# Optimization experiments

Hardware: AMD Instinct MI355X
Metric: run time of the kernel (lower is better)

The kernel has to match this reference:

```python
import jax, jax.numpy as jnp
import numpy as np

INPUT_DIM = 1024
UNITS = 1024

def setup_inputs() -> dict:
    key = jax.random.key(0)
    ks = jax.random.split(key, 7)
    B, S = 4, 2048
    x = jax.random.normal(ks[0], (B, S, INPUT_DIM), dtype=jnp.float32)
    # nn.Linear weights stored as [out, in]; biases [out]
    scale = 1.0 / np.sqrt(INPUT_DIM)
    Wq = jax.random.uniform(ks[1], (UNITS, INPUT_DIM), jnp.float32, -scale, scale)
    bq = jax.random.uniform(ks[2], (UNITS,), jnp.float32, -scale, scale)
    Wk = jax.random.uniform(ks[3], (UNITS, INPUT_DIM), jnp.float32, -scale, scale)
    bk = jax.random.uniform(ks[4], (UNITS,), jnp.float32, -scale, scale)
    Wv = jax.random.uniform(ks[5], (UNITS, INPUT_DIM), jnp.float32, -scale, scale)
    bv = jax.random.uniform(ks[6], (UNITS,), jnp.float32, -scale, scale)
    return {"x": x, "Wq": Wq, "bq": bq, "Wk": Wk, "bk": bk, "Wv": Wv, "bv": bv}

def reference(x, Wq, bq, Wk, bk, Wv, bv):
    # Q/K/V projections: [B,S,D] @ [D,U]
    Q = jnp.einsum('bsd,ud->bsu', x, Wq) + bq
    K = jnp.einsum('bsd,ud->bsu', x, Wk) + bk
    V = jnp.einsum('bsd,ud->bsu', x, Wv) + bv
    scores = jnp.einsum('bqu,bku->bqk', Q, K) / jnp.sqrt(jnp.float32(UNITS))
    attn = jax.nn.softmax(scores, axis=-1)
    return jnp.einsum('bqk,bku->bqu', attn, V)
```

## Files before the change

kernel.cpp:

```cpp
#include <hip/hip_runtime.h>
#include <cstdint>
#include <cstddef>


typedef unsigned short ushort_t;
typedef __attribute__((ext_vector_type(8))) short short8;
typedef __attribute__((ext_vector_type(4))) float f32x4;

#define AS1 __attribute__((address_space(1)))
#define AS3 __attribute__((address_space(3)))

__device__ __forceinline__ ushort_t f2bf(float f) {
    unsigned int u = __float_as_uint(f);
    u += 0x7FFFu + ((u >> 16) & 1u);
    return (ushort_t)(u >> 16);
}
__device__ __forceinline__ float bf2f(ushort_t b) {
    return __uint_as_float(((unsigned)b) << 16);
}

__device__ __forceinline__ void async_ld16(const void* g, unsigned lds_off) {
    __builtin_amdgcn_global_load_lds((const AS1 void*)(uintptr_t)g,
                                     (AS3 void*)(uintptr_t)lds_off,
                                     16, 0, 0);
}

template <int N>
__device__ __forceinline__ void wait_vmcnt() {
    if constexpr (N == 0)      asm volatile("s_waitcnt vmcnt(0)" ::: "memory");
    else if constexpr (N == 4) asm volatile("s_waitcnt vmcnt(4)" ::: "memory");
    else                       asm volatile("s_waitcnt vmcnt(6)" ::: "memory");
}

template <typename OT, int EPI, int BN>
__global__ __launch_bounds__(512, 2) void gemm8(
    const ushort_t* __restrict__ A, const ushort_t* __restrict__ B,
    const float* __restrict__ bias0, const float* __restrict__ bias1,
    OT* __restrict__ C, int K, int lda, int ldb, int ldc, float scale,
    long long aOffZ, long long bOffZ, long long cOffZ)
{
    constexpr int NJ   = BN / 64;
    constexpr int NBH  = (BN == 256) ? 2 : 1;
    constexpr int VPRO = (BN == 256) ? 6 : 4;

    __shared__ __align__(16) ushort_t As[2][2][128 * 64];
    __shared__ __align__(16) ushort_t Bs[2][NBH][128 * 64];
    __shared__ float rs[256];

    const int tid  = threadIdx.x;
    const int wave = tid >> 6;
    const int lane = tid & 63;

    A += (size_t)blockIdx.z * aOffZ;
    B += (size_t)blockIdx.z * bOffZ;

    const int m0 = blockIdx.y * 256;
    const int n0 = blockIdx.x * BN;
    const int g  = wave >> 2;
    const int wm = g * 128;
    const int wn = (wave & 3) * (BN / 4);

    const int srow = wave * 8 + (lane >> 3);
    const int cd   = ((lane & 7) - srow) & 7;
    const unsigned lw = (unsigned)(wave << 10);

    const ushort_t* Ast = A + (size_t)(m0 + srow) * lda + cd * 8;
    const ushort_t* Bst = B + (size_t)(n0 + srow) * ldb + cd * 8;

    unsigned aB[2][2], bB[2][NBH];
#pragma unroll
    for (int b2 = 0; b2 < 2; ++b2) {
        aB[b2][0] = (unsigned)(uintptr_t)&As[b2][0][0];
        aB[b2][1] = (unsigned)(uintptr_t)&As[b2][1][0];
#pragma unroll
        for (int h = 0; h < NBH; ++h)
            bB[b2][h] = (unsigned)(uintptr_t)&Bs[b2][h][0];
    }

    auto stA = [&](int t, int rsel) {
        const int buf = t & 1;
        const int k0  = t << 6;
        async_ld16(Ast + (size_t)(rsel * 64) * lda + k0,
                   aB[buf][0] + (unsigned)(rsel * 8192) + lw);
        async_ld16(Ast + (size_t)(rsel * 64 + 128) * lda + k0,
                   aB[buf][1] + (unsigned)(rsel * 8192) + lw);
    };
    auto stB = [&](int t, int h) {
        const int buf = t & 1;
        const int k0  = t << 6;
        async_ld16(Bst + (size_t)(h * 128) * ldb + k0, bB[buf][h] + lw);
        async_ld16(Bst + (size_t)(h * 128 + 64) * ldb + k0,
                   bB[buf][h] + 8192 + lw);
    };

    const int frow = lane & 15;
    const int fg   = lane >> 4;
    const int hB   = (BN == 256) ? (wn >> 7) : 0;

    const int NT = K >> 6;

    f32x4 acc[8][NJ] = {};
    float rsacc[8] = {};
    short8 bfr[NJ][2];

    stB(0, 0);
    if (BN == 256) stB(0, 1);
    stA(0, 0); stA(0, 1);
    stB(1, 0);
    if (BN == 256) stB(1, 1);
    stA(1, 0);
    wait_vmcnt<VPRO>();
    __builtin_amdgcn_s_barrier();

    for (int t = 0; t < NT; ++t) {
        const int buf = t & 1;
        const ushort_t* Aw = &As[buf][g][0];
        const ushort_t* Bw = &Bs[buf][hB][0];
#pragma unroll
        for (int ph = 0; ph < 4; ++ph) {
            short8 af[2][2];
#pragma unroll
            for (int di = 0; di < 2; ++di) {
                const int r = (ph * 2 + di) * 16 + frow;
#pragma unroll
                for (int kk = 0; kk < 2; ++kk)
                    af[di][kk] = *(const short8*)
                        &Aw[r * 64 + (((kk << 2) + fg + r) & 7) * 8];
            }
            if (ph == 0) {
#pragma unroll
                for (int j = 0; j < NJ; ++j) {
                    const int rb = (wn & 127) + j * 16 + frow;
#pragma unroll
                    for (int kk = 0; kk < 2; ++kk)
                        bfr[j][kk] = *(const short8*)
                            &Bw[rb * 64 + (((kk << 2) + fg + rb) & 7) * 8];
                }
                if (t + 1 < NT) stA(t + 1, 1);
            }
            if (ph == 1 && t + 2 < NT) stB(t + 2, 0);
            if (ph == 2 && t + 2 < NT) {
                if (BN == 256) stB(t + 2, 1);
                else           stA(t + 2, 0);
            }
            if (ph == 3) {
                if (BN == 256 && t + 2 < NT) stA(t + 2, 0);
                if (t + 2 < NT)      wait_vmcnt<VPRO>();
                else if (t + 1 < NT) wait_vmcnt<0>();
            }
            __builtin_amdgcn_s_barrier();
            asm volatile("s_waitcnt lgkmcnt(0)" ::: "memory");
            __builtin_amdgcn_s_setprio(1);
#pragma unroll
            for (int di = 0; di < 2; ++di)
#pragma unroll
                for (int j = 0; j < NJ; ++j)
#pragma unroll
                    for (int kk = 0; kk < 2; ++kk)
                        acc[ph * 2 + di][j] =
                            __builtin_amdgcn_mfma_f32_16x16x32_bf16(
                                af[di][kk], bfr[j][kk],
                                acc[ph * 2 + di][j], 0, 0, 0);
            __builtin_amdgcn_s_setprio(0);
            if (EPI == 4 && wn == 0) {
#pragma unroll
                for (int di = 0; di < 2; ++di)
#pragma unroll
                    for (int kk = 0; kk < 2; ++kk)
#pragma unroll
                        for (int e = 0; e < 8; ++e)
                            rsacc[ph * 2 + di] += bf2f((ushort_t)af[di][kk][e]);
            }
            __builtin_amdgcn_s_barrier();
        }
    }

    if (EPI == 4) {
        if (wn == 0) {
#pragma unroll
            for (int i = 0; i < 8; ++i) {
                float s = rsacc[i];
                s += __shfl_xor(s, 16, 64);
                s += __shfl_xor(s, 32, 64);
                rs[wm + i * 16 + frow] = s;
            }
        }
        __syncthreads();
    }

    C += (size_t)blockIdx.z * cOffZ;
    const int r0 = fg << 2;
    const int c0 = lane & 15;
#pragma unroll
    for (int i = 0; i < 8; ++i) {
        float bm[4];
        if (EPI == 2) {
#pragma unroll
            for (int r = 0; r < 4; ++r)
                bm[r] = bias0[m0 + wm + i * 16 + r0 + r];
        }
        if (EPI == 4) {
#pragma unroll
            for (int r = 0; r < 4; ++r)
                bm[r] = 1.0f / rs[wm + i * 16 + r0 + r];
        }
#pragma unroll
        for (int j = 0; j < NJ; ++j) {
            const int n = n0 + wn + j * 16 + c0;
            float bn = 0.f;
            if (EPI == 1) bn = (n < 1024) ? bias0[n] : bias1[n - 1024];
#pragma unroll
            for (int r = 0; r < 4; ++r) {
                const int m = m0 + wm + i * 16 + r0 + r;
                float v = acc[i][j][r] * scale;
                if (EPI == 1) v += bn;
                if (EPI == 2) v += bm[r];
                if (EPI == 3) v = __expf(v);
                if (EPI == 4) v *= bm[r];
                if constexpr (sizeof(OT) == 2)
                    C[(size_t)m * ldc + n] = f2bf(v);
                else
                    C[(size_t)m * ldc + n] = v;
            }
        }
    }
}

__global__ __launch_bounds__(256) void cvt_all(
    const float* __restrict__ x,  const float* __restrict__ wq,
    const float* __restrict__ wk, const float* __restrict__ wv,
    ushort_t* __restrict__ xb,  ushort_t* __restrict__ wqb,
    ushort_t* __restrict__ wkb, ushort_t* __restrict__ wvb)
{
    const int b = blockIdx.x;
    const float* src; ushort_t* dst; size_t base;
    if (b < 4096)      { src = x;  dst = xb;  base = (size_t)b * 2048; }
    else if (b < 4608) { src = wq; dst = wqb; base = (size_t)(b - 4096) * 2048; }
    else if (b < 5120) { src = wk; dst = wkb; base = (size_t)(b - 4608) * 2048; }
    else               { src = wv; dst = wvb; base = (size_t)(b - 5120) * 2048; }
    const size_t i = base + threadIdx.x * 8;
    const f32x4 a = *(const f32x4*)(src + i);
    const f32x4 c = *(const f32x4*)(src + i + 4);
    short8 o;
    o[0] = (short)f2bf(a[0]); o[1] = (short)f2bf(a[1]);
    o[2] = (short)f2bf(a[2]); o[3] = (short)f2bf(a[3]);
    o[4] = (short)f2bf(c[0]); o[5] = (short)f2bf(c[1]);
    o[6] = (short)f2bf(c[2]); o[7] = (short)f2bf(c[3]);
    *(short8*)(dst + i) = o;
}

extern "C" void kernel_launch(void* const* d_in, const int* in_sizes, int n_in,
                              void* d_out, int out_size, void* d_ws, size_t ws_size,
                              hipStream_t stream)
{
    const float* x  = (const float*)d_in[0];
    const float* Wq = (const float*)d_in[1];
    const float* bq = (const float*)d_in[2];
    const float* Wk = (const float*)d_in[3];
    const float* bk = (const float*)d_in[4];
    const float* Wv = (const float*)d_in[5];
    const float* bv = (const float*)d_in[6];
    float* out = (float*)d_out;

    char* ws = (char*)d_ws;
    const size_t MB = 1ull << 20;
    ushort_t* Xb   = (ushort_t*)(ws);
    ushort_t* Wqkb = (ushort_t*)(ws + 16 * MB);
    ushort_t* Wkb  = (ushort_t*)(ws + 18 * MB);
    ushort_t* Wvb  = (ushort_t*)(ws + 20 * MB);
    ushort_t* QKb  = (ushort_t*)(ws + 32 * MB);
    ushort_t* Vt   = (ushort_t*)(ws + 64 * MB);
    ushort_t* Sc   = (ushort_t*)(ws);

    cvt_all<<<dim3(5632), dim3(256), 0, stream>>>(
        x, Wq, Wk, Wv, Xb, Wqkb, Wkb, Wvb);

    gemm8<ushort_t, 1, 256><<<dim3(8, 32, 1), dim3(512), 0, stream>>>(
        Xb, Wqkb, bq, bk, QKb, 1024, 1024, 1024, 2048, 1.0f, 0, 0, 0);

    gemm8<ushort_t, 2, 128><<<dim3(64, 4, 1), dim3(512), 0, stream>>>(
        Wvb, Xb, bv, nullptr, Vt, 1024, 1024, 1024, 8192, 1.0f, 0, 0, 0);

    gemm8<ushort_t, 3, 256><<<dim3(8, 8, 4), dim3(512), 0, stream>>>(
        QKb, QKb + 1024, nullptr, nullptr, Sc, 1024, 2048, 2048, 2048,
        0.03125f, 2048ll * 2048, 2048ll * 2048, 2048ll * 2048);

    gemm8<float, 4, 128><<<dim3(8, 8, 4), dim3(512), 0, stream>>>(
        Sc, Vt, nullptr, nullptr, out, 2048, 2048, 8192, 1024, 1.0f,
        2048ll * 2048, 2048ll, 2048ll * 1024);
}
```

Baseline: 259.5 us.

## Remap GEMM tiles into XCD-local chunks and halve phases for BN=128

Block indices are remapped so that consecutive blocks landing on the same XCD (bid & 7) cover a compact CX×CY tile region, which should improve L2 reuse of A/B panels on the chiplet-based MI355X. For BN=128 kernels the inner k-loop now runs 2 phases with 4 row-fragments each instead of 4 phases with 2, with both prefetch loads issued in phase 1. This halves the barrier count per k-step for those kernels but concentrates the global-load issue into one phase and raises fragment register pressure.

```diff
diff --git a/kernel.cpp b/kernel.cpp
--- a/kernel.cpp
+++ b/kernel.cpp
@@ -32,7 +32,7 @@
     else                       asm volatile("s_waitcnt vmcnt(6)" ::: "memory");
 }
 
-template <typename OT, int EPI, int BN>
+template <typename OT, int EPI, int BN, int CX, int CY>
 __global__ __launch_bounds__(512, 2) void gemm8(
     const ushort_t* __restrict__ A, const ushort_t* __restrict__ B,
     const float* __restrict__ bias0, const float* __restrict__ bias1,
@@ -42,6 +42,9 @@
     constexpr int NJ   = BN / 64;
     constexpr int NBH  = (BN == 256) ? 2 : 1;
     constexpr int VPRO = (BN == 256) ? 6 : 4;
+    constexpr int NPH  = (BN == 256) ? 4 : 2;
+    constexpr int DPP  = 8 / NPH;
+    constexpr int CZ   = 32 / (CX * CY);
 
     __shared__ __align__(16) ushort_t As[2][2][128 * 64];
     __shared__ __align__(16) ushort_t Bs[2][NBH][128 * 64];
@@ -51,11 +54,22 @@
     const int wave = tid >> 6;
     const int lane = tid & 63;
 
-    A += (size_t)blockIdx.z * aOffZ;
-    B += (size_t)blockIdx.z * bOffZ;
-
-    const int m0 = blockIdx.y * 256;
-    const int n0 = blockIdx.x * BN;
+    const int GX  = gridDim.x, GY = gridDim.y;
+    const int bid = blockIdx.x + GX * (blockIdx.y + GY * blockIdx.z);
+    const int xcd = bid & 7;
+    const int jj  = bid >> 3;
+    const int NCX = GX / CX, NCY = GY / CY;
+    const int cx  = xcd % NCX, ctt = xcd / NCX;
+    const int cy  = ctt % NCY, cz  = ctt / NCY;
+    const int bx  = cx * CX + (jj % CX);
+    const int by  = cy * CY + ((jj / CX) % CY);
+    const int bz  = cz * CZ + jj / (CX * CY);
+
+    A += (size_t)bz * aOffZ;
+    B += (size_t)bz * bOffZ;
+
+    const int m0 = by * 256;
+    const int n0 = bx * BN;
     const int g  = wave >> 2;
     const int wm = g * 128;
     const int wn = (wave & 3) * (BN / 4);
@@ -117,11 +131,11 @@
         const ushort_t* Aw = &As[buf][g][0];
         const ushort_t* Bw = &Bs[buf][hB][0];
 #pragma unroll
-        for (int ph = 0; ph < 4; ++ph) {
-            short8 af[2][2];
-#pragma unroll
-            for (int di = 0; di < 2; ++di) {
-                const int r = (ph * 2 + di) * 16 + frow;
+        for (int ph = 0; ph < NPH; ++ph) {
+            short8 af[DPP][2];
+#pragma unroll
+            for (int di = 0; di < DPP; ++di) {
+                const int r = (ph * DPP + di) * 16 + frow;
 #pragma unroll
                 for (int kk = 0; kk < 2; ++kk)
                     af[di][kk] = *(const short8*)
@@ -138,38 +152,43 @@
                 }
                 if (t + 1 < NT) stA(t + 1, 1);
             }
-            if (ph == 1 && t + 2 < NT) stB(t + 2, 0);
-            if (ph == 2 && t + 2 < NT) {
-                if (BN == 256) stB(t + 2, 1);
-                else           stA(t + 2, 0);
-            }
-            if (ph == 3) {
-                if (BN == 256 && t + 2 < NT) stA(t + 2, 0);
-                if (t + 2 < NT)      wait_vmcnt<VPRO>();
-                else if (t + 1 < NT) wait_vmcnt<0>();
+            if (NPH == 4) {
+                if (ph == 1 && t + 2 < NT) stB(t + 2, 0);
+                if (ph == 2 && t + 2 < NT) stB(t + 2, 1);
+                if (ph == 3) {
+                    if (t + 2 < NT)      { stA(t + 2, 0); wait_vmcnt<VPRO>(); }
+                    else if (t + 1 < NT) wait_vmcnt<0>();
+                }
+            } else {
+                if (ph == 1) {
+                    if (t + 2 < NT) { stB(t + 2, 0); stA(t + 2, 0);
+                                      wait_vmcnt<VPRO>(); }
+                    else if (t + 1 < NT) wait_vmcnt<0>();
+                }
             }
             __builtin_amdgcn_s_barrier();
             asm volatile("s_waitcnt lgkmcnt(0)" ::: "memory");
             __builtin_amdgcn_s_setprio(1);
 #pragma unroll
-            for (int di = 0; di < 2; ++di)
+            for (int di = 0; di < DPP; ++di)
 #pragma unroll
                 for (int j = 0; j < NJ; ++j)
 #pragma unroll
                     for (int kk = 0; kk < 2; ++kk)
-                        acc[ph * 2 + di][j] =
+                        acc[ph * DPP + di][j] =
                             __builtin_amdgcn_mfma_f32_16x16x32_bf16(
                                 af[di][kk], bfr[j][kk],
-                                acc[ph * 2 + di][j], 0, 0, 0);
+                                acc[ph * DPP + di][j], 0, 0, 0);
             __builtin_amdgcn_s_setprio(0);
             if (EPI == 4 && wn == 0) {
 #pragma unroll
-                for (int di = 0; di < 2; ++di)
+                for (int di = 0; di < DPP; ++di)
 #pragma unroll
                     for (int kk = 0; kk < 2; ++kk)
 #pragma unroll
                         for (int e = 0; e < 8; ++e)
-                            rsacc[ph * 2 + di] += bf2f((ushort_t)af[di][kk][e]);
+                            rsacc[ph * DPP + di] +=
+                                bf2f((ushort_t)af[di][kk][e]);
             }
             __builtin_amdgcn_s_barrier();
         }
@@ -188,7 +207,7 @@
         __syncthreads();
     }
 
-    C += (size_t)blockIdx.z * cOffZ;
+    C += (size_t)bz * cOffZ;
     const int r0 = fg << 2;
     const int c0 = lane & 15;
 #pragma unroll
@@ -266,26 +285,25 @@
     const size_t MB = 1ull << 20;
     ushort_t* Xb   = (ushort_t*)(ws);
     ushort_t* Wqkb = (ushort_t*)(ws + 16 * MB);
-    ushort_t* Wkb  = (ushort_t*)(ws + 18 * MB);
     ushort_t* Wvb  = (ushort_t*)(ws + 20 * MB);
     ushort_t* QKb  = (ushort_t*)(ws + 32 * MB);
     ushort_t* Vt   = (ushort_t*)(ws + 64 * MB);
     ushort_t* Sc   = (ushort_t*)(ws);
 
     cvt_all<<<dim3(5632), dim3(256), 0, stream>>>(
-        x, Wq, Wk, Wv, Xb, Wqkb, Wkb, Wvb);
-
-    gemm8<ushort_t, 1, 256><<<dim3(8, 32, 1), dim3(512), 0, stream>>>(
+        x, Wq, Wk, Wv, Xb, Wqkb, (ushort_t*)(ws + 18 * MB), Wvb);
+
+    gemm8<ushort_t, 1, 256, 4, 8><<<dim3(8, 32, 1), dim3(512), 0, stream>>>(
         Xb, Wqkb, bq, bk, QKb, 1024, 1024, 1024, 2048, 1.0f, 0, 0, 0);
 
-    gemm8<ushort_t, 2, 128><<<dim3(64, 4, 1), dim3(512), 0, stream>>>(
+    gemm8<ushort_t, 2, 128, 8, 4><<<dim3(64, 4, 1), dim3(512), 0, stream>>>(
         Wvb, Xb, bv, nullptr, Vt, 1024, 1024, 1024, 8192, 1.0f, 0, 0, 0);
 
-    gemm8<ushort_t, 3, 256><<<dim3(8, 8, 4), dim3(512), 0, stream>>>(
+    gemm8<ushort_t, 3, 256, 4, 8><<<dim3(8, 8, 4), dim3(512), 0, stream>>>(
         QKb, QKb + 1024, nullptr, nullptr, Sc, 1024, 2048, 2048, 2048,
         0.03125f, 2048ll * 2048, 2048ll * 2048, 2048ll * 2048);
 
-    gemm8<float, 4, 128><<<dim3(8, 8, 4), dim3(512), 0, stream>>>(
+    gemm8<float, 4, 128, 8, 4><<<dim3(8, 8, 4), dim3(512), 0, stream>>>(
         Sc, Vt, nullptr, nullptr, out, 2048, 2048, 8192, 1024, 1.0f,
         2048ll * 2048, 2048ll, 2048ll * 1024);
 }
```

Measured after the change: 257.1 us. No clear change (-0.9%).
